# Performance work log

Hardware: AMD Instinct MI355X
Metric: run time of the kernel (lower is better)

Reference implementation:

```python
import jax, jax.numpy as jnp
import numpy as np

N = 20000
E = 320000
H = 16
C = 16
NUM_GRAPHS = 64
NEG_SLOPE = 0.2


def _gat(x, edge_index, W, a_src, a_dst, bias):
    # PyG GATConv, concat=True, shared lin for src/dst, eval mode (no dropout)
    h = (x @ W).reshape(-1, H, C)                       # [N,H,C]
    src, dst = edge_index[0], edge_index[1]
    alpha_src = jnp.sum(h * a_src, axis=-1)             # [N,H]
    alpha_dst = jnp.sum(h * a_dst, axis=-1)             # [N,H]
    alpha = alpha_src[src] + alpha_dst[dst]             # [E,H]
    alpha = jax.nn.leaky_relu(alpha, NEG_SLOPE)
    amax = jax.ops.segment_max(alpha, dst, num_segments=N)
    ex = jnp.exp(alpha - amax[dst])
    denom = jax.ops.segment_sum(ex, dst, num_segments=N)
    attn = ex / jnp.where(denom == 0, 1.0, denom)[dst]  # [E,H]
    msg = h[src] * attn[:, :, None]                     # [E,H,C]
    out = jax.ops.segment_sum(msg, dst, num_segments=N) # [N,H,C]
    return out.reshape(-1, H * C) + bias


def setup_inputs() -> dict:
    key = jax.random.key(0)
    ks = jax.random.split(key, 32)
    d = {}
    d['x'] = jax.random.normal(ks[0], (N, 20), dtype=jnp.float32)
    d['edge_index_ipv6'] = jax.random.randint(ks[1], (2, E), 0, N)
    d['edge_attr_ipv6'] = jax.random.normal(ks[2], (E, 19), dtype=jnp.float32)
    d['edge_index_tsch'] = jax.random.randint(ks[3], (2, E), 0, N)
    d['edge_attr_tsch'] = jax.random.normal(ks[4], (E, 7), dtype=jnp.float32)
    d['batch'] = jnp.sort(jax.random.randint(ks[5], (N,), 0, NUM_GRAPHS))
    s = 0.1
    d['W_i'] = jax.random.normal(ks[6], (20, H * C), dtype=jnp.float32) * s
    d['a_src_i'] = jax.random.normal(ks[7], (H, C), dtype=jnp.float32) * s
    d['a_dst_i'] = jax.random.normal(ks[8], (H, C), dtype=jnp.float32) * s
    d['b_i'] = jnp.zeros((H * C,), dtype=jnp.float32)
    d['W_t'] = jax.random.normal(ks[9], (20, H * C), dtype=jnp.float32) * s
    d['a_src_t'] = jax.random.normal(ks[10], (H, C), dtype=jnp.float32) * s
    d['a_dst_t'] = jax.random.normal(ks[11], (H, C), dtype=jnp.float32) * s
    d['b_t'] = jnp.zeros((H * C,), dtype=jnp.float32)
    d['Wf'] = jax.random.normal(ks[12], (512, 64), dtype=jnp.float32) * s
    d['bf'] = jnp.zeros((64,), dtype=jnp.float32)
    d['W1'] = jax.random.normal(ks[13], (64, 32), dtype=jnp.float32) * s
    d['b1'] = jnp.zeros((32,), dtype=jnp.float32)
    d['W2'] = jax.random.normal(ks[14], (32, 16), dtype=jnp.float32) * s
    d['b2'] = jnp.zeros((16,), dtype=jnp.float32)
    d['W3'] = jax.random.normal(ks[15], (16, 16), dtype=jnp.float32) * s
    d['b3'] = jnp.zeros((16,), dtype=jnp.float32)
    d['Wce'] = jax.random.normal(ks[16], (16, 3), dtype=jnp.float32) * s
    d['bce'] = jnp.zeros((3,), dtype=jnp.float32)
    d['Wcv'] = jax.random.normal(ks[17], (16, 3), dtype=jnp.float32) * s
    d['bcv'] = jnp.zeros((3,), dtype=jnp.float32)
    return d


def reference(x, edge_index_ipv6, edge_attr_ipv6, edge_index_tsch, edge_attr_tsch,
              batch, W_i, a_src_i, a_dst_i, b_i, W_t, a_src_t, a_dst_t, b_t,
              Wf, bf, W1, b1, W2, b2, W3, b3, Wce, bce, Wcv, bcv):
    # edge_attr_* are ignored by GATConv (edge_dim=None in PyG), as in original
    n_ipv6 = _gat(x, edge_index_ipv6, W_i, a_src_i, a_dst_i, b_i)
    n_tsch = _gat(x, edge_index_tsch, W_t, a_src_t, a_dst_t, b_t)
    h = jnp.concatenate([n_ipv6, n_tsch], axis=-1)      # [N,512]
    h = jax.nn.relu(h @ Wf + bf)
    h = jax.nn.relu(h @ W1 + b1)
    h = jax.nn.relu(h @ W2 + b2)
    h = jax.nn.relu(h @ W3 + b3)                        # [N,16]
    ssum = jax.ops.segment_sum(h, batch, num_segments=NUM_GRAPHS)
    cnt = jax.ops.segment_sum(jnp.ones((h.shape[0], 1), h.dtype), batch,
                              num_segments=NUM_GRAPHS)
    g = ssum / jnp.where(cnt == 0, 1.0, cnt)            # [G,16]
    out_event = g @ Wce + bce
    out_env = g @ Wcv + bcv
    return out_event, out_env
```

## Files before the change

kernel.cpp:

```cpp
#include <hip/hip_runtime.h>
#include <math.h>

#define N_NODES 20000
#define N_EDGES 320000
#define NG 64
#define NEG 0.2f
#define NCHUNK ((N_NODES + 255) / 256)
#define FLAGBIT (1 << 30)

typedef __attribute__((ext_vector_type(8))) short bf16x8;
typedef __attribute__((ext_vector_type(4))) float f32x4;

__device__ __forceinline__ unsigned short f2bf(float f) {
  unsigned int u = __float_as_uint(f);
  return (unsigned short)((u + 0x7fffu + ((u >> 16) & 1u)) >> 16);
}
__device__ __forceinline__ unsigned int pk2bf(float a, float b) {
  return (unsigned int)f2bf(a) | ((unsigned int)f2bf(b) << 16);
}

__global__ __launch_bounds__(256) void k_front(
    const float* __restrict__ x,
    const float* __restrict__ W_i, const float* __restrict__ as_i, const float* __restrict__ ad_i,
    const float* __restrict__ W_t, const float* __restrict__ as_t, const float* __restrict__ ad_t,
    const float* __restrict__ Wf, const float* __restrict__ bf,
    const float* __restrict__ b_i, const float* __restrict__ b_t,
    const int* __restrict__ ei0, const int* __restrict__ ei1,
    unsigned short* __restrict__ wbigfrag, float* __restrict__ bfold,
    unsigned short* __restrict__ xpadbf,
    float* __restrict__ asrc0, float* __restrict__ adst0,
    float* __restrict__ asrc1, float* __restrict__ adst1,
    int* __restrict__ fill0, int* __restrict__ fill1) {
  __shared__ float bred[4][64];
  __shared__ float xs[16][20];
  __shared__ float ws[20][64];
  int b = blockIdx.x, t = threadIdx.x;
  if (b < 160) {
    int idx = b * 256 + t;
    int ct = idx / 10240, rem = idx % 10240;
    int lane = (rem >> 3) & 63, j = rem & 7, ks = rem >> 9;
    int k = ks * 32 + ((lane >> 4) << 3) + j;
    int nc = ct * 16 + (lane & 15);
    int g = (k >= 320) ? 1 : 0;
    int r = k - g * 320;
    int ch = r >> 4, h = r & 15;
    float v = 0.f;
    if (ch < 20) {
      const float* W = g ? W_t : W_i;
      const float* wr = W + ch * 256 + (h << 4);
      const float* wf = Wf + ((g << 8) + (h << 4)) * 64 + nc;
#pragma unroll
      for (int m = 0; m < 16; ++m) v = fmaf(wr[m], wf[m * 64], v);
    }
    wbigfrag[idx] = f2bf(v);
    return;
  }
  if (b == 160) {
    int wv = t >> 6, j = t & 63;
    float p = 0.f;
    int i0 = wv * 128;
#pragma unroll 4
    for (int i = i0; i < i0 + 128; ++i) {
      float bb = (i < 256) ? b_i[i] : b_t[i - 256];
      p = fmaf(bb, Wf[i * 64 + j], p);
    }
    bred[wv][j] = p;
    __syncthreads();
    if (wv == 0) bfold[j] = bred[0][j] + bred[1][j] + bred[2][j] + bred[3][j] + bf[j];
    return;
  }
  int a = b - 161;
  int e = a * 256 + t;
  int d0 = ei0[N_EDGES + e];
  int d1 = ei1[N_EDGES + e];
  atomicAdd(&fill0[d0], 1);
  atomicAdd(&fill1[d1], 1);
  int n0 = a * 16;
  for (int i = t; i < 320; i += 256) {
    int nd = i / 20, k = i % 20;
    xs[nd][k] = x[(n0 + nd) * 20 + k];
  }
  for (int i = t; i < 1280; i += 256) {
    int k = i >> 6, c = i & 63;
    int set = c >> 5, role = (c >> 4) & 1, h = c & 15;
    const float* W = set ? W_t : W_i;
    const float* av = set ? (role ? ad_t : as_t) : (role ? ad_i : as_i);
    float v = 0.f;
#pragma unroll
    for (int j = 0; j < 16; ++j) v = fmaf(W[k * 256 + h * 16 + j], av[h * 16 + j], v);
    ws[k][c] = v;
  }
  __syncthreads();
  for (int i = t; i < 512; i += 256) {
    int nd = i >> 5, j = i & 31;
    float v = (j < 20) ? xs[nd][j] : (j == 20 ? 1.f : 0.f);
    xpadbf[(size_t)(n0 + nd) * 32 + j] = f2bf(v);
  }
#pragma unroll
  for (int i = 0; i < 4; ++i) {
    int wi = i * 256 + t;
    int nd = wi >> 6, c = wi & 63;
    float v = 0.f;
#pragma unroll
    for (int k = 0; k < 20; ++k) v = fmaf(xs[nd][k], ws[k][c], v);
    int n = n0 + nd, h = c & 15;
    float* arr = (c >> 5) ? ((c >> 4) & 1 ? adst1 : asrc1)
                          : ((c >> 4) & 1 ? adst0 : asrc0);
    arr[n * 16 + h] = v;
  }
}

__global__ __launch_bounds__(256) void k_scan(
    int* __restrict__ fill0, int* __restrict__ fill1,
    int* __restrict__ rp0, int* __restrict__ rp1,
    int* __restrict__ aggs) {
  int chunk = blockIdx.x, set = blockIdx.y;
  int* fill = set ? fill1 : fill0;
  int* rp = set ? rp1 : rp0;
  int t = threadIdx.x, lane = t & 63, wv = t >> 6;
  int i = chunk * 256 + t;
  int v = (i < N_NODES) ? fill[i] : 0;
  int s = v;
#pragma unroll
  for (int d = 1; d < 64; d <<= 1) {
    int o = __shfl_up(s, d);
    if (lane >= d) s += o;
  }
  __shared__ int wsum[4];
  if (lane == 63) wsum[wv] = s;
  __syncthreads();
  int pre = 0;
#pragma unroll
  for (int j = 0; j < 4; ++j)
    if (j < wv) pre += wsum[j];
  s += pre;
  int agg = wsum[0] + wsum[1] + wsum[2] + wsum[3];
  if (t == 0)
    __hip_atomic_store(&aggs[set * 128 + chunk], agg | FLAGBIT,
                       __ATOMIC_RELEASE, __HIP_MEMORY_SCOPE_AGENT);
  __shared__ int reds[256];
  int part = 0;
  for (int j = t; j < chunk; j += 256) {
    int a;
    do {
      a = __hip_atomic_load(&aggs[set * 128 + j], __ATOMIC_ACQUIRE,
                            __HIP_MEMORY_SCOPE_AGENT);
    } while (!(a & FLAGBIT));
    part += a & (FLAGBIT - 1);
  }
  reds[t] = part;
  __syncthreads();
  for (int st = 128; st > 0; st >>= 1) {
    if (t < st) reds[t] += reds[t + st];
    __syncthreads();
  }
  int carry = reds[0];
  int excl = carry + s - v;
  if (i < N_NODES) {
    rp[i] = excl;
    fill[i] = excl;
    if (i == N_NODES - 1) rp[N_NODES] = excl + v;
  }
}

__global__ void k_scatter(const int* __restrict__ ei0, const int* __restrict__ ei1,
                          int* __restrict__ fill0, int* __restrict__ fill1,
                          unsigned short* __restrict__ srcs0,
                          unsigned short* __restrict__ srcs1) {
  int e = blockIdx.x * blockDim.x + threadIdx.x;
  if (e >= N_EDGES) return;
  const int* ei = blockIdx.y ? ei1 : ei0;
  int* fill = blockIdx.y ? fill1 : fill0;
  unsigned short* srcs = blockIdx.y ? srcs1 : srcs0;
  int d = ei[N_EDGES + e];
  int pos = atomicAdd(&fill[d], 1);
  srcs[pos] = (unsigned short)ei[e];
}

__global__ __launch_bounds__(256) void k_gatmlp(
    const unsigned short* __restrict__ xpadbf,
    const float* __restrict__ asrc0, const float* __restrict__ adst0,
    const float* __restrict__ asrc1, const float* __restrict__ adst1,
    const int* __restrict__ rp0, const unsigned short* __restrict__ srcs0,
    const int* __restrict__ rp1, const unsigned short* __restrict__ srcs1,
    unsigned short* __restrict__ xagg, const unsigned short* __restrict__ wbigfrag,
    const float* __restrict__ bfold,
    const float* __restrict__ W1m, const float* __restrict__ b1v,
    const float* __restrict__ W2m, const float* __restrict__ b2v,
    const float* __restrict__ W3m, const float* __restrict__ b3v,
    const int* __restrict__ batch,
    float* __restrict__ gsum, int* __restrict__ gcnt) {
  __shared__ __align__(16) char smem_[15360];
  int t = threadIdx.x;
  int w4 = t >> 6, lane = t & 63;
  int n0 = blockIdx.x * 16;

  {
    int eid = lane & 15, slot = lane >> 4;
    int h16 = lane & 15, e8 = (lane >> 4) * 8;
    unsigned short* ext = (unsigned short*)smem_ + w4 * 640;
    unsigned short* xtw = (unsigned short*)(smem_ + 5120) + w4 * 1280;
    int g = w4 & 1;
    const float* asrc = g ? asrc1 : asrc0;
    const float* adst = g ? adst1 : adst0;
    const int* rp = g ? rp1 : rp0;
    const unsigned short* srcs = g ? srcs1 : srcs0;
    for (int it = 0; it < 8; ++it) {
      int n = n0 + it * 2 + (w4 >> 1);
      int k0 = rp[n], k1 = rp[n + 1];
      const float4 adn4 = *(const float4*)&adst[n * 16 + slot * 4];
      f32x4 acc0 = {0.f, 0.f, 0.f, 0.f}, acc1 = acc0;
      for (int base = k0; base < k1; base += 32) {
        int e0 = base + 2 * eid, e1 = e0 + 1;
        int sa = (int)srcs[min(e0, k1 - 1)];
        int sbb = (int)srcs[min(e1, k1 - 1)];
        const float4 ava = *(const float4*)&asrc[sa * 16 + slot * 4];
        const float4 avb = *(const float4*)&asrc[sbb * 16 + slot * 4];
        const uint4 xra = *(const uint4*)&xpadbf[(size_t)sa * 32 + slot * 8];
        const uint4 xrb = *(const uint4*)&xpadbf[(size_t)sbb * 32 + slot * 8];
        float ea[4], eb[4];
        {
          float a;
          bool v0 = e0 < k1, v1 = e1 < k1;
          a = ava.x + adn4.x; a = a >= 0.f ? a : NEG * a; ea[0] = v0 ? __expf(a) : 0.f;
          a = ava.y + adn4.y; a = a >= 0.f ? a : NEG * a; ea[1] = v0 ? __expf(a) : 0.f;
          a = ava.z + adn4.z; a = a >= 0.f ? a : NEG * a; ea[2] = v0 ? __expf(a) : 0.f;
          a = ava.w + adn4.w; a = a >= 0.f ? a : NEG * a; ea[3] = v0 ? __expf(a) : 0.f;
          a = avb.x + adn4.x; a = a >= 0.f ? a : NEG * a; eb[0] = v1 ? __expf(a) : 0.f;
          a = avb.y + adn4.y; a = a >= 0.f ? a : NEG * a; eb[1] = v1 ? __expf(a) : 0.f;
          a = avb.z + adn4.z; a = a >= 0.f ? a : NEG * a; eb[2] = v1 ? __expf(a) : 0.f;
          a = avb.w + adn4.w; a = a >= 0.f ? a : NEG * a; eb[3] = v1 ? __expf(a) : 0.f;
        }
#pragma unroll
        for (int r = 0; r < 4; ++r)
          *(unsigned int*)&ext[(slot * 4 + r) * 40 + 2 * eid] = pk2bf(ea[r], eb[r]);
        unsigned int ua[4] = {xra.x, xra.y, xra.z, xra.w};
        unsigned int ub[4] = {xrb.x, xrb.y, xrb.z, xrb.w};
#pragma unroll
        for (int q = 0; q < 8; ++q) {
          unsigned int baq = (q & 1) ? (ua[q >> 1] >> 16) : (ua[q >> 1] & 0xffffu);
          unsigned int bbq = (q & 1) ? (ub[q >> 1] >> 16) : (ub[q >> 1] & 0xffffu);
          int ch = slot * 8 + q;
          *(unsigned int*)&xtw[(ch >> 4) * 640 + (ch & 15) * 40 + 2 * eid] =
              baq | (bbq << 16);
        }
        bf16x8 A = *(const bf16x8*)&ext[h16 * 40 + e8];
        bf16x8 B0 = *(const bf16x8*)&xtw[h16 * 40 + e8];
        bf16x8 B1 = *(const bf16x8*)&xtw[640 + h16 * 40 + e8];
        acc0 = __builtin_amdgcn_mfma_f32_16x16x32_bf16(A, B0, acc0, 0, 0, 0);
        acc1 = __builtin_amdgcn_mfma_f32_16x16x32_bf16(A, B1, acc1, 0, 0, 0);
      }
      float inv[4];
#pragma unroll
      for (int r = 0; r < 4; ++r) {
        float dr = __shfl(acc1[r], (lane & 48) | 4);
        inv[r] = dr > 0.f ? 1.f / dr : 0.f;
      }
      int ss = lane >> 4, c = lane & 15;
      size_t nb = (size_t)n * 640 + g * 320;
      uint2 o0;
      o0.x = pk2bf(acc0[0] * inv[0], acc0[1] * inv[1]);
      o0.y = pk2bf(acc0[2] * inv[2], acc0[3] * inv[3]);
      *(uint2*)&xagg[nb + c * 16 + ss * 4] = o0;
      if (c < 4) {
        uint2 o1v;
        o1v.x = pk2bf(acc1[0] * inv[0], acc1[1] * inv[1]);
        o1v.y = pk2bf(acc1[2] * inv[2], acc1[3] * inv[3]);
        *(uint2*)&xagg[nb + 256 + c * 16 + ss * 4] = o1v;
      }
    }
  }
  __syncthreads();

  {
    float* o1 = (float*)smem_;
    float* o2 = o1 + 1088;
    float* o3 = o2 + 576;
    float* o4 = o3 + 320;
    int* bs = (int*)(o4 + 272);
    if (t < 16) bs[t] = batch[n0 + t];
    int w = w4;
    {
      int m = lane & 15, kb = lane >> 4;
      const unsigned short* aptr = xagg + (size_t)(n0 + m) * 640 + kb * 8;
      const unsigned short* bbase = wbigfrag + (size_t)w * 10240 + lane * 8;
      f32x4 acc = {0.f, 0.f, 0.f, 0.f};
#pragma unroll 5
      for (int ks = 0; ks < 20; ++ks) {
        bf16x8 af = *(const bf16x8*)(aptr + ks * 32);
        bf16x8 bfr = *(const bf16x8*)(bbase + (size_t)ks * 512);
        acc = __builtin_amdgcn_mfma_f32_16x16x32_bf16(af, bfr, acc, 0, 0, 0);
      }
      int col = lane & 15, rg = lane >> 4;
#pragma unroll
      for (int r = 0; r < 4; ++r) {
        int row = rg * 4 + r;
        o1[row * 68 + w * 16 + col] = fmaxf(acc[r] + bfold[w * 16 + col], 0.f);
      }
    }
    __syncthreads();
    int nd = t >> 4, js = t & 15;
    {
      float a0 = b1v[js], a1 = b1v[js + 16];
#pragma unroll 8
      for (int k = 0; k < 64; ++k) {
        float hv = o1[nd * 68 + k];
        a0 = fmaf(hv, W1m[k * 32 + js], a0);
        a1 = fmaf(hv, W1m[k * 32 + js + 16], a1);
      }
      o2[nd * 36 + js] = fmaxf(a0, 0.f);
      o2[nd * 36 + js + 16] = fmaxf(a1, 0.f);
    }
    __syncthreads();
    {
      float a = b2v[js];
#pragma unroll
      for (int k = 0; k < 32; ++k) a = fmaf(o2[nd * 36 + k], W2m[k * 16 + js], a);
      o3[nd * 20 + js] = fmaxf(a, 0.f);
    }
    __syncthreads();
    {
      float a = b3v[js];
#pragma unroll
      for (int k = 0; k < 16; ++k) a = fmaf(o3[nd * 20 + k], W3m[k * 16 + js], a);
      o4[nd * 17 + js] = fmaxf(a, 0.f);
    }
    __syncthreads();
    if (t < 128) {
      int s = t >> 4, jx = t & 15;
      int b = bs[0] + s;
      if (b <= bs[15]) {
        float sum = 0.f; int c = 0;
#pragma unroll
        for (int ndd = 0; ndd < 16; ++ndd)
          if (bs[ndd] == b) { sum += o4[ndd * 17 + jx]; ++c; }
        if (c > 0) {
          atomicAdd(&gsum[b * 16 + jx], sum);
          if (jx == 0) atomicAdd(&gcnt[b], c);
        }
      }
    }
  }
}

__global__ void k_head(const float* __restrict__ gsum, const int* __restrict__ gcnt,
                       const float* __restrict__ Wce, const float* __restrict__ bce,
                       const float* __restrict__ Wcv, const float* __restrict__ bcv,
                       float* __restrict__ out) {
  int t = threadIdx.x;
  if (t >= 384) return;
  int half = t / 192, idx = t % 192;
  int b = idx / 3, r = idx % 3;
  float cnt = (float)gcnt[b];
  float inv = cnt > 0.f ? 1.f / cnt : 1.f;
  const float* Wc = half ? Wcv : Wce;
  const float* bc = half ? bcv : bce;
  float v = bc[r];
#pragma unroll
  for (int j = 0; j < 16; ++j) v = fmaf(gsum[b * 16 + j] * inv, Wc[j * 3 + r], v);
  out[t] = v;
}

extern "C" void kernel_launch(void* const* d_in, const int* in_sizes, int n_in,
                              void* d_out, int out_size, void* d_ws, size_t ws_size,
                              hipStream_t stream) {
  const float* x = (const float*)d_in[0];
  const int* ei_i = (const int*)d_in[1];
  const int* ei_t = (const int*)d_in[3];
  const int* batch = (const int*)d_in[5];
  const float* W_i = (const float*)d_in[6];
  const float* as_i = (const float*)d_in[7];
  const float* ad_i = (const float*)d_in[8];
  const float* b_i = (const float*)d_in[9];
  const float* W_t = (const float*)d_in[10];
  const float* as_t = (const float*)d_in[11];
  const float* ad_t = (const float*)d_in[12];
  const float* b_t = (const float*)d_in[13];
  const float* Wf = (const float*)d_in[14];
  const float* bf = (const float*)d_in[15];
  const float* W1 = (const float*)d_in[16];
  const float* b1 = (const float*)d_in[17];
  const float* W2 = (const float*)d_in[18];
  const float* b2 = (const float*)d_in[19];
  const float* W3 = (const float*)d_in[20];
  const float* b3 = (const float*)d_in[21];
  const float* Wce = (const float*)d_in[22];
  const float* bce = (const float*)d_in[23];
  const float* Wcv = (const float*)d_in[24];
  const float* bcv = (const float*)d_in[25];

  char* ws = (char*)d_ws;
  size_t off = 0;
  auto take = [&](size_t bytes) {
    void* p = ws + off;
    off = (off + bytes + 255) & ~(size_t)255;
    return p;
  };
  unsigned short* xpadbf = (unsigned short*)take((size_t)N_NODES * 32 * 2);
  unsigned short* xagg = (unsigned short*)take((size_t)N_NODES * 640 * 2);
  unsigned short* wbigfrag = (unsigned short*)take((size_t)40960 * 2);
  float* bfold = (float*)take((size_t)64 * 4);
  float* asrc_i = (float*)take((size_t)N_NODES * 16 * 4);
  float* adst_i = (float*)take((size_t)N_NODES * 16 * 4);
  float* asrc_t = (float*)take((size_t)N_NODES * 16 * 4);
  float* adst_t = (float*)take((size_t)N_NODES * 16 * 4);
  int* rowptr_i = (int*)take((size_t)(N_NODES + 1) * 4);
  int* rowptr_t = (int*)take((size_t)(N_NODES + 1) * 4);
  unsigned short* srcs_i = (unsigned short*)take((size_t)N_EDGES * 2);
  unsigned short* srcs_t = (unsigned short*)take((size_t)N_EDGES * 2);
  int zero_ints = N_NODES + N_NODES + NG * 16 + NG + 256;
  int* fill_i = (int*)take((size_t)zero_ints * 4);
  int* fill_t = fill_i + N_NODES;
  float* gsum = (float*)(fill_t + N_NODES);
  int* gcnt = (int*)(gsum + NG * 16);
  int* csums = gcnt + NG;

  hipMemsetAsync(fill_i, 0, (size_t)zero_ints * 4, stream);

  k_front<<<1411, 256, 0, stream>>>(x, W_i, as_i, ad_i, W_t, as_t, ad_t,
                                    Wf, bf, b_i, b_t, ei_i, ei_t,
                                    wbigfrag, bfold, xpadbf,
                                    asrc_i, adst_i, asrc_t, adst_t,
                                    fill_i, fill_t);

  dim3 sgrid(NCHUNK, 2);
  k_scan<<<sgrid, 256, 0, stream>>>(fill_i, fill_t, rowptr_i, rowptr_t, csums);

  dim3 egrid((N_EDGES + 255) / 256, 2);
  k_scatter<<<egrid, 256, 0, stream>>>(ei_i, ei_t, fill_i, fill_t, srcs_i, srcs_t);

  k_gatmlp<<<N_NODES / 16, 256, 0, stream>>>(
      xpadbf, asrc_i, adst_i, asrc_t, adst_t,
      rowptr_i, srcs_i, rowptr_t, srcs_t,
      xagg, wbigfrag, bfold, W1, b1, W2, b2, W3, b3,
      batch, gsum, gcnt);

  k_head<<<1, 384, 0, stream>>>(gsum, gcnt, Wce, bce, Wcv, bcv, (float*)d_out);
}
```

Before: 133.6 us.

## Software-pipeline neighbor gathers across destination nodes in GAT aggregation

Loads row pointers once per wave via a lane register and shuffles, then prefetches all first-chunk source indices for the 8 nodes up front. The gathers of asrc, adst and x rows for the next node are issued before the current node's compute, to hide dependent gather latency. This adds register pressure from the prefetched float4/uint4 values and index arrays, which may lower occupancy.

```diff
diff --git a/kernel.cpp b/kernel.cpp
--- a/kernel.cpp
+++ b/kernel.cpp
@@ -197,58 +197,94 @@
 
   {
     int eid = lane & 15, slot = lane >> 4;
-    int h16 = lane & 15, e8 = (lane >> 4) * 8;
-    unsigned short* ext = (unsigned short*)smem_ + w4 * 640;
-    unsigned short* xtw = (unsigned short*)(smem_ + 5120) + w4 * 1280;
+    int h16 = lane & 15, e8 = slot * 8;
+    int half = w4 >> 1;
     int g = w4 & 1;
     const float* asrc = g ? asrc1 : asrc0;
     const float* adst = g ? adst1 : adst0;
     const int* rp = g ? rp1 : rp0;
     const unsigned short* srcs = g ? srcs1 : srcs0;
+    unsigned short* ext = (unsigned short*)smem_ + w4 * 640;
+    unsigned short* xtw = (unsigned short*)(smem_ + 5120) + w4 * 1280;
+
+    auto COMPUTE = [&](f32x4& a0, f32x4& a1, const float4& adn4,
+                       const float4& ava, const float4& avb,
+                       const uint4& xra, const uint4& xrb, int base, int k1) {
+      float ea[4], eb[4];
+      bool v0 = (base + 2 * eid) < k1, v1 = (base + 2 * eid + 1) < k1;
+      float a;
+      a = ava.x + adn4.x; a = a >= 0.f ? a : NEG * a; ea[0] = v0 ? __expf(a) : 0.f;
+      a = ava.y + adn4.y; a = a >= 0.f ? a : NEG * a; ea[1] = v0 ? __expf(a) : 0.f;
+      a = ava.z + adn4.z; a = a >= 0.f ? a : NEG * a; ea[2] = v0 ? __expf(a) : 0.f;
+      a = ava.w + adn4.w; a = a >= 0.f ? a : NEG * a; ea[3] = v0 ? __expf(a) : 0.f;
+      a = avb.x + adn4.x; a = a >= 0.f ? a : NEG * a; eb[0] = v1 ? __expf(a) : 0.f;
+      a = avb.y + adn4.y; a = a >= 0.f ? a : NEG * a; eb[1] = v1 ? __expf(a) : 0.f;
+      a = avb.z + adn4.z; a = a >= 0.f ? a : NEG * a; eb[2] = v1 ? __expf(a) : 0.f;
+      a = avb.w + adn4.w; a = a >= 0.f ? a : NEG * a; eb[3] = v1 ? __expf(a) : 0.f;
+#pragma unroll
+      for (int r = 0; r < 4; ++r)
+        *(unsigned int*)&ext[(slot * 4 + r) * 40 + 2 * eid] = pk2bf(ea[r], eb[r]);
+      unsigned int ua[4] = {xra.x, xra.y, xra.z, xra.w};
+      unsigned int ub[4] = {xrb.x, xrb.y, xrb.z, xrb.w};
+#pragma unroll
+      for (int q = 0; q < 8; ++q) {
+        unsigned int baq = (q & 1) ? (ua[q >> 1] >> 16) : (ua[q >> 1] & 0xffffu);
+        unsigned int bbq = (q & 1) ? (ub[q >> 1] >> 16) : (ub[q >> 1] & 0xffffu);
+        int ch = slot * 8 + q;
+        *(unsigned int*)&xtw[(ch >> 4) * 640 + (ch & 15) * 40 + 2 * eid] =
+            baq | (bbq << 16);
+      }
+      bf16x8 A = *(const bf16x8*)&ext[h16 * 40 + e8];
+      bf16x8 B0 = *(const bf16x8*)&xtw[h16 * 40 + e8];
+      bf16x8 B1 = *(const bf16x8*)&xtw[640 + h16 * 40 + e8];
+      a0 = __builtin_amdgcn_mfma_f32_16x16x32_bf16(A, B0, a0, 0, 0, 0);
+      a1 = __builtin_amdgcn_mfma_f32_16x16x32_bf16(A, B1, a1, 0, 0, 0);
+    };
+
+    int rpv = (lane < 17) ? rp[n0 + lane] : 0;
+    int sa[8], sb[8];
+#pragma unroll
     for (int it = 0; it < 8; ++it) {
-      int n = n0 + it * 2 + (w4 >> 1);
-      int k0 = rp[n], k1 = rp[n + 1];
-      const float4 adn4 = *(const float4*)&adst[n * 16 + slot * 4];
+      int k0 = __shfl(rpv, it * 2 + half);
+      int k1 = __shfl(rpv, it * 2 + half + 1);
+      int last = k1 - 1; if (last < k0) last = k0;
+      int e0 = k0 + 2 * eid;
+      sa[it] = (int)srcs[min(e0, last)];
+      sb[it] = (int)srcs[min(e0 + 1, last)];
+    }
+    float4 adnC = *(const float4*)&adst[(n0 + half) * 16 + slot * 4];
+    float4 avaC = *(const float4*)&asrc[sa[0] * 16 + slot * 4];
+    float4 avbC = *(const float4*)&asrc[sb[0] * 16 + slot * 4];
+    uint4 xraC = *(const uint4*)&xpadbf[(size_t)sa[0] * 32 + slot * 8];
+    uint4 xrbC = *(const uint4*)&xpadbf[(size_t)sb[0] * 32 + slot * 8];
+
+#pragma unroll
+    for (int it = 0; it < 8; ++it) {
+      float4 adnN, avaN, avbN;
+      uint4 xraN, xrbN;
+      if (it + 1 < 8) {
+        adnN = *(const float4*)&adst[(n0 + (it + 1) * 2 + half) * 16 + slot * 4];
+        avaN = *(const float4*)&asrc[sa[it + 1] * 16 + slot * 4];
+        avbN = *(const float4*)&asrc[sb[it + 1] * 16 + slot * 4];
+        xraN = *(const uint4*)&xpadbf[(size_t)sa[it + 1] * 32 + slot * 8];
+        xrbN = *(const uint4*)&xpadbf[(size_t)sb[it + 1] * 32 + slot * 8];
+      }
+      int n = n0 + it * 2 + half;
+      int k0 = __shfl(rpv, it * 2 + half);
+      int k1 = __shfl(rpv, it * 2 + half + 1);
       f32x4 acc0 = {0.f, 0.f, 0.f, 0.f}, acc1 = acc0;
-      for (int base = k0; base < k1; base += 32) {
-        int e0 = base + 2 * eid, e1 = e0 + 1;
-        int sa = (int)srcs[min(e0, k1 - 1)];
-        int sbb = (int)srcs[min(e1, k1 - 1)];
-        const float4 ava = *(const float4*)&asrc[sa * 16 + slot * 4];
-        const float4 avb = *(const float4*)&asrc[sbb * 16 + slot * 4];
-        const uint4 xra = *(const uint4*)&xpadbf[(size_t)sa * 32 + slot * 8];
-        const uint4 xrb = *(const uint4*)&xpadbf[(size_t)sbb * 32 + slot * 8];
-        float ea[4], eb[4];
-        {
-          float a;
-          bool v0 = e0 < k1, v1 = e1 < k1;
-          a = ava.x + adn4.x; a = a >= 0.f ? a : NEG * a; ea[0] = v0 ? __expf(a) : 0.f;
-          a = ava.y + adn4.y; a = a >= 0.f ? a : NEG * a; ea[1] = v0 ? __expf(a) : 0.f;
-          a = ava.z + adn4.z; a = a >= 0.f ? a : NEG * a; ea[2] = v0 ? __expf(a) : 0.f;
-          a = ava.w + adn4.w; a = a >= 0.f ? a : NEG * a; ea[3] = v0 ? __expf(a) : 0.f;
-          a = avb.x + adn4.x; a = a >= 0.f ? a : NEG * a; eb[0] = v1 ? __expf(a) : 0.f;
-          a = avb.y + adn4.y; a = a >= 0.f ? a : NEG * a; eb[1] = v1 ? __expf(a) : 0.f;
-          a = avb.z + adn4.z; a = a >= 0.f ? a : NEG * a; eb[2] = v1 ? __expf(a) : 0.f;
-          a = avb.w + adn4.w; a = a >= 0.f ? a : NEG * a; eb[3] = v1 ? __expf(a) : 0.f;
+      if (k1 > k0) {
+        COMPUTE(acc0, acc1, adnC, avaC, avbC, xraC, xrbC, k0, k1);
+        for (int base = k0 + 32; base < k1; base += 32) {
+          int e0 = base + 2 * eid, e1 = e0 + 1;
+          int s2a = (int)srcs[min(e0, k1 - 1)];
+          int s2b = (int)srcs[min(e1, k1 - 1)];
+          float4 av2a = *(const float4*)&asrc[s2a * 16 + slot * 4];
+          float4 av2b = *(const float4*)&asrc[s2b * 16 + slot * 4];
+          uint4 xr2a = *(const uint4*)&xpadbf[(size_t)s2a * 32 + slot * 8];
+          uint4 xr2b = *(const uint4*)&xpadbf[(size_t)s2b * 32 + slot * 8];
+          COMPUTE(acc0, acc1, adnC, av2a, av2b, xr2a, xr2b, base, k1);
         }
-#pragma unroll
-        for (int r = 0; r < 4; ++r)
-          *(unsigned int*)&ext[(slot * 4 + r) * 40 + 2 * eid] = pk2bf(ea[r], eb[r]);
-        unsigned int ua[4] = {xra.x, xra.y, xra.z, xra.w};
-        unsigned int ub[4] = {xrb.x, xrb.y, xrb.z, xrb.w};
-#pragma unroll
-        for (int q = 0; q < 8; ++q) {
-          unsigned int baq = (q & 1) ? (ua[q >> 1] >> 16) : (ua[q >> 1] & 0xffffu);
-          unsigned int bbq = (q & 1) ? (ub[q >> 1] >> 16) : (ub[q >> 1] & 0xffffu);
-          int ch = slot * 8 + q;
-          *(unsigned int*)&xtw[(ch >> 4) * 640 + (ch & 15) * 40 + 2 * eid] =
-              baq | (bbq << 16);
-        }
-        bf16x8 A = *(const bf16x8*)&ext[h16 * 40 + e8];
-        bf16x8 B0 = *(const bf16x8*)&xtw[h16 * 40 + e8];
-        bf16x8 B1 = *(const bf16x8*)&xtw[640 + h16 * 40 + e8];
-        acc0 = __builtin_amdgcn_mfma_f32_16x16x32_bf16(A, B0, acc0, 0, 0, 0);
-        acc1 = __builtin_amdgcn_mfma_f32_16x16x32_bf16(A, B1, acc1, 0, 0, 0);
       }
       float inv[4];
 #pragma unroll
@@ -256,18 +292,18 @@
         float dr = __shfl(acc1[r], (lane & 48) | 4);
         inv[r] = dr > 0.f ? 1.f / dr : 0.f;
       }
-      int ss = lane >> 4, c = lane & 15;
       size_t nb = (size_t)n * 640 + g * 320;
       uint2 o0;
       o0.x = pk2bf(acc0[0] * inv[0], acc0[1] * inv[1]);
       o0.y = pk2bf(acc0[2] * inv[2], acc0[3] * inv[3]);
-      *(uint2*)&xagg[nb + c * 16 + ss * 4] = o0;
-      if (c < 4) {
+      *(uint2*)&xagg[nb + eid * 16 + slot * 4] = o0;
+      if (eid < 4) {
         uint2 o1v;
         o1v.x = pk2bf(acc1[0] * inv[0], acc1[1] * inv[1]);
         o1v.y = pk2bf(acc1[2] * inv[2], acc1[3] * inv[3]);
-        *(uint2*)&xagg[nb + 256 + c * 16 + ss * 4] = o1v;
-      }
+        *(uint2*)&xagg[nb + 256 + eid * 16 + slot * 4] = o1v;
+      }
+      adnC = adnN; avaC = avaN; avbC = avbN; xraC = xraN; xrbC = xrbN;
     }
   }
   __syncthreads();
@@ -278,12 +314,13 @@
     float* o3 = o2 + 576;
     float* o4 = o3 + 320;
     int* bs = (int*)(o4 + 272);
+    int lane2 = t & 63;
     if (t < 16) bs[t] = batch[n0 + t];
     int w = w4;
     {
-      int m = lane & 15, kb = lane >> 4;
+      int m = lane2 & 15, kb = lane2 >> 4;
       const unsigned short* aptr = xagg + (size_t)(n0 + m) * 640 + kb * 8;
-      const unsigned short* bbase = wbigfrag + (size_t)w * 10240 + lane * 8;
+      const unsigned short* bbase = wbigfrag + (size_t)w * 10240 + lane2 * 8;
       f32x4 acc = {0.f, 0.f, 0.f, 0.f};
 #pragma unroll 5
       for (int ks = 0; ks < 20; ++ks) {
@@ -291,7 +328,7 @@
         bf16x8 bfr = *(const bf16x8*)(bbase + (size_t)ks * 512);
         acc = __builtin_amdgcn_mfma_f32_16x16x32_bf16(af, bfr, acc, 0, 0, 0);
       }
-      int col = lane & 15, rg = lane >> 4;
+      int col = lane2 & 15, rg = lane2 >> 4;
 #pragma unroll
       for (int r = 0; r < 4; ++r) {
         int row = rg * 4 + r;
```

Result: slower. 136.8 us (+2.4%).
